# Kernel tuning notes

Hardware: AMD Instinct MI355X
Metric: run time of the kernel (lower is better)

The kernel has to match this reference:

```python
import jax, jax.numpy as jnp
import numpy as np

B, L, D, H, NL, EXP = 8, 1024, 512, 8, 6, 4
DH = D // H
DF = D * EXP
EPS = 1e-3  # keras LayerNormalization default epsilon
NEG = -1e9  # keras Softmax mask adder for float32


def _ln(x, g, b):
    m = jnp.mean(x, axis=-1, keepdims=True)
    v = jnp.mean(jnp.square(x - m), axis=-1, keepdims=True)
    return (x - m) * jax.lax.rsqrt(v + EPS) * g + b


def _pos_emb(L, D):
    pos = jnp.arange(L, dtype=jnp.float32)[:, None]          # [L,1]
    i = jnp.arange(D // 2, dtype=jnp.float32)[None, :]        # [1,D/2]
    inv = jnp.power(10000.0, -2.0 * i / D)
    # original concatenates sin block then cos block along feature axis
    return jnp.concatenate([jnp.sin(pos * inv), jnp.cos(pos * inv)], axis=-1)  # [L,D]


def setup_inputs() -> dict:
    key = jax.random.key(0)
    ks = jax.random.split(key, 16)
    glorot = lambda k, shape: jax.random.uniform(
        k, shape, jnp.float32, -1.0, 1.0) * jnp.sqrt(6.0 / (shape[-2] + shape[-1]))
    return {
        "x": jax.random.normal(ks[0], (B, L, D), jnp.float32),
        "lengths": jax.random.randint(ks[1], (B,), L // 2, L + 1).astype(jnp.int32),
        "Wq": glorot(ks[2], (NL, D, D)),
        "Wk": glorot(ks[3], (NL, D, D)),
        "Wv": glorot(ks[4], (NL, D, D)),
        "Wo": glorot(ks[5], (NL, D, D)),
        "ln1_g": jnp.ones((NL, D), jnp.float32),
        "ln1_b": jnp.zeros((NL, D), jnp.float32),
        "ln2_g": jnp.ones((NL, D), jnp.float32),
        "ln2_b": jnp.zeros((NL, D), jnp.float32),
        "w1": glorot(ks[6], (NL, D, DF)),
        "b1": jnp.zeros((NL, DF), jnp.float32),
        "w2": glorot(ks[7], (NL, DF, D)),
        "b2": jnp.zeros((NL, D), jnp.float32),
    }


def _forward(x, mask_bias, Wq, Wk, Wv, Wo, ln1_g, ln1_b, ln2_g, ln2_b, w1, b1, w2, b2):
    x = x + _pos_emb(L, D)[None, :, :]
    scale = 1.0 / jnp.sqrt(jnp.float32(DH))

    def layer(x, p):
        wq, wk, wv, wo, g1, be1, g2, be2, fw1, fb1, fw2, fb2 = p
        h = _ln(x, g1, be1)
        split = lambda t: t.reshape(B, L, H, DH).transpose(0, 2, 1, 3)  # [B,H,L,DH]
        q, k, v = split(h @ wq), split(h @ wk), split(h @ wv)
        scores = jnp.einsum("bhqd,bhkd->bhqk", q, k) * scale + mask_bias
        attn = jax.nn.softmax(scores, axis=-1)
        o = jnp.einsum("bhqk,bhkd->bhqd", attn, v)
        o = o.transpose(0, 2, 1, 3).reshape(B, L, D) @ wo
        x = x + o  # dropout is identity at inference
        h2 = _ln(x, g2, be2)
        ffn = jax.nn.relu(h2 @ fw1 + fb1) @ fw2 + fb2
        return x + ffn, None

    x, _ = jax.lax.scan(layer, x, (Wq, Wk, Wv, Wo, ln1_g, ln1_b, ln2_g, ln2_b, w1, b1, w2, b2))
    return x


def reference(x, lengths, Wq, Wk, Wv, Wo, ln1_g, ln1_b, ln2_g, ln2_b, w1, b1, w2, b2):
    mask = (jnp.arange(L)[None, :] < lengths[:, None]).astype(jnp.float32)  # [B,L]
    mask_bias = (1.0 - mask)[:, None, None, :] * NEG                        # [B,1,1,L]
    return _forward(x, mask_bias, Wq, Wk, Wv, Wo, ln1_g, ln1_b, ln2_g, ln2_b, w1, b1, w2, b2)
```

## Files before the change

### kernel.cpp

```cpp
#include <hip/hip_runtime.h>
#include <cstdint>
#include <cstddef>

#define Bz 8
#define Lz 1024
#define Dz 512
#define Hz 8
#define NLz 6
#define DFz 2048
#define Mz (Bz*Lz)

typedef short bf16x8 __attribute__((ext_vector_type(8)));
typedef float f32x4  __attribute__((ext_vector_type(4)));

__device__ __forceinline__ short f2bf(float f) {
    unsigned u = __builtin_bit_cast(unsigned, f);
    u = (u + 0x7fff + ((u >> 16) & 1)) >> 16;
    return (short)u;
}

__device__ __forceinline__ float exp2_fast(float x) {
#if __has_builtin(__builtin_amdgcn_exp2f)
    return __builtin_amdgcn_exp2f(x);
#else
    return exp2f(x);
#endif
}

#define GLD16(gp, lp) __builtin_amdgcn_global_load_lds( \
    (const __attribute__((address_space(1))) void*)(gp), \
    (__attribute__((address_space(3))) void*)(lp), 16, 0, 0)

__global__ __launch_bounds__(256) void posadd_kernel(const float* __restrict__ x,
                                                     float* __restrict__ y) {
    int idx = blockIdx.x * 256 + threadIdx.x;
    int d   = idx & (Dz - 1);
    int pos = (idx >> 9) & (Lz - 1);
    int i2  = (d < Dz/2) ? d : d - Dz/2;
    float inv = __expf(-0.03597789207f * (float)i2);
    float a = (float)pos * inv;
    float pe = (d < Dz/2) ? sinf(a) : cosf(a);
    y[idx] = x[idx] + pe;
}

__global__ __launch_bounds__(256) void ln_kernel(const float* __restrict__ x,
                                                 const float* __restrict__ g,
                                                 const float* __restrict__ b,
                                                 short* __restrict__ out) {
    int row = blockIdx.x;
    int t = threadIdx.x;
    const float* xr = x + (size_t)row * Dz;
    float v0 = xr[t], v1 = xr[t + 256];
    float s = v0 + v1;
    #pragma unroll
    for (int off = 32; off; off >>= 1) s += __shfl_xor(s, off, 64);
    __shared__ float red[4];
    int w = t >> 6, l = t & 63;
    if (l == 0) red[w] = s;
    __syncthreads();
    float m = (red[0] + red[1] + red[2] + red[3]) * (1.0f / Dz);
    float d0 = v0 - m, d1 = v1 - m;
    float s2 = d0 * d0 + d1 * d1;
    #pragma unroll
    for (int off = 32; off; off >>= 1) s2 += __shfl_xor(s2, off, 64);
    __syncthreads();
    if (l == 0) red[w] = s2;
    __syncthreads();
    float var = (red[0] + red[1] + red[2] + red[3]) * (1.0f / Dz);
    float rs = rsqrtf(var + 1e-3f);
    out[(size_t)row * Dz + t]       = f2bf(d0 * rs * g[t] + b[t]);
    out[(size_t)row * Dz + t + 256] = f2bf(d1 * rs * g[t + 256] + b[t + 256]);
}

__global__ __launch_bounds__(256) void transpose_bf16_kernel(const float* __restrict__ src,
                                                             short* __restrict__ dst,
                                                             int K, int N,
                                                             long srcLS, long dstLS, int rowOff) {
    __shared__ float tile[32][33];
    int tx = threadIdx.x & 31, ty = threadIdx.x >> 5;
    int bx = blockIdx.x, by = blockIdx.y, z = blockIdx.z;
    const float* s = src + (size_t)z * srcLS;
    short* d = dst + (size_t)z * dstLS;
    #pragma unroll
    for (int i = 0; i < 4; i++)
        tile[ty + i * 8][tx] = s[(size_t)(by * 32 + ty + i * 8) * N + bx * 32 + tx];
    __syncthreads();
    #pragma unroll
    for (int i = 0; i < 4; i++)
        d[(size_t)(rowOff + bx * 32 + ty + i * 8) * K + by * 32 + tx] = f2bf(tile[tx][ty + i * 8]);
}

__global__ __launch_bounds__(256) void vtrans_kernel(const short* __restrict__ qkv,
                                                     short* __restrict__ vbt) {
    int lt = blockIdx.x, bh = blockIdx.y;
    int b = bh >> 3, h = bh & 7;
    __shared__ short tile[64][72];
    int t = threadIdx.x;
    int l = t >> 2, c4 = t & 3;
    #pragma unroll
    for (int p = 0; p < 2; p++) {
        int dd = (c4 + p * 4) * 8;
        *(uint4*)&tile[l][dd] =
            *(const uint4*)(qkv + ((size_t)(b * Lz + lt * 64 + l)) * 1536 + 1024 + h * 64 + dd);
    }
    __syncthreads();
    int d = t >> 2;
    #pragma unroll
    for (int p = 0; p < 2; p++) {
        int lc = (c4 + p * 4) * 8;
        union { uint4 u; short s[8]; } o;
        #pragma unroll
        for (int j = 0; j < 8; j++) o.s[j] = tile[lc + j][d];
        *(uint4*)(vbt + ((size_t)(bh * 64 + d)) * Lz + lt * 64 + lc) = o.u;
    }
}

template<int MODE, int TN>
__global__ __launch_bounds__(256, (TN == 64) ? 4 : 2)
void gemm_bt(const short* __restrict__ A,
             const short* __restrict__ Bt,
             short* __restrict__ outb,
             float* __restrict__ outf,
             const float* __restrict__ bias,
             int M, int N, int K) {
    constexpr int NI = TN / 32;
    __shared__ __attribute__((aligned(16))) short As[128 * 32];
    __shared__ __attribute__((aligned(16))) short Bs[TN * 32];
    int t = threadIdx.x;
    int m0 = blockIdx.x * 128, n0 = blockIdx.y * TN;
    int w = t >> 6, l = t & 63;
    int wm = (w >> 1) * 64, wn = (w & 1) * (TN / 2);
    int lr = l & 15, lq = l >> 4;
    f32x4 acc[4][NI] = {};
    int ra0 = t >> 2, ca0 = (t & 3) * 8;
    int ra1 = (t + 256) >> 2;
    for (int kk = 0; kk < K; kk += 32) {
        GLD16(A + (size_t)(m0 + ra0) * K + kk + ca0, As + t * 8);
        GLD16(A + (size_t)(m0 + ra1) * K + kk + ca0, As + (t + 256) * 8);
        GLD16(Bt + (size_t)(n0 + ra0) * K + kk + ca0, Bs + t * 8);
        if constexpr (TN == 128)
            GLD16(Bt + (size_t)(n0 + ra1) * K + kk + ca0, Bs + (t + 256) * 8);
        __syncthreads();
        bf16x8 af[4], bfr[NI];
        #pragma unroll
        for (int i = 0; i < 4; i++)  af[i]  = *(const bf16x8*)(As + (wm + i * 16 + lr) * 32 + lq * 8);
        #pragma unroll
        for (int i = 0; i < NI; i++) bfr[i] = *(const bf16x8*)(Bs + (wn + i * 16 + lr) * 32 + lq * 8);
        #pragma unroll
        for (int mi = 0; mi < 4; mi++)
            #pragma unroll
            for (int ni = 0; ni < NI; ni++)
                acc[mi][ni] = __builtin_amdgcn_mfma_f32_16x16x32_bf16(af[mi], bfr[ni], acc[mi][ni], 0, 0, 0);
        __syncthreads();
    }
    #pragma unroll
    for (int mi = 0; mi < 4; mi++)
        #pragma unroll
        for (int ni = 0; ni < NI; ni++) {
            int col = n0 + wn + ni * 16 + lr;
            float bv = (MODE == 2 || MODE == 3) ? bias[col] : 0.0f;
            #pragma unroll
            for (int r = 0; r < 4; r++) {
                int row = m0 + wm + mi * 16 + lq * 4 + r;
                size_t idx = (size_t)row * N + col;
                float v = acc[mi][ni][r];
                if (MODE == 0)      outb[idx] = f2bf(v);
                else if (MODE == 1) outf[idx] += v;
                else if (MODE == 2) outb[idx] = f2bf(fmaxf(v + bv, 0.0f));
                else                outf[idx] += v + bv;
            }
        }
}

__device__ __forceinline__ void attn_frag(f32x4* sacc, const float* biask,
                                          float* mr, float* lsum, f32x4* oacc,
                                          short* Pw, const short* Vs,
                                          int lr, int lq, bf16x8 onesf) {
    const float SC2 = 0.18033688f;
    float p[8][4];
    #pragma unroll
    for (int r = 0; r < 4; r++) {
        float mx = -1e30f;
        #pragma unroll
        for (int kt = 0; kt < 8; kt++) {
            p[kt][r] = sacc[kt][r] * SC2 + biask[kt];
            mx = fmaxf(mx, p[kt][r]);
        }
        mx = fmaxf(mx, __shfl_xor(mx, 1, 64));
        mx = fmaxf(mx, __shfl_xor(mx, 2, 64));
        mx = fmaxf(mx, __shfl_xor(mx, 4, 64));
        mx = fmaxf(mx, __shfl_xor(mx, 8, 64));
        float mn = fmaxf(mr[r], mx);
        float alpha = exp2_fast(mr[r] - mn);
        mr[r] = mn;
        #pragma unroll
        for (int kt = 0; kt < 8; kt++)
            p[kt][r] = exp2_fast(p[kt][r] - mn);
        lsum[r] *= alpha;
        #pragma unroll
        for (int ni = 0; ni < 4; ni++) oacc[ni][r] *= alpha;
    }
    #pragma unroll
    for (int kt = 0; kt < 8; kt++)
        #pragma unroll
        for (int r = 0; r < 4; r++)
            Pw[(lq * 4 + r) * 136 + kt * 16 + lr] = f2bf(p[kt][r]);
    f32x4 sums = {};
    #pragma unroll
    for (int c = 0; c < 4; c++) {
        bf16x8 pf = *(const bf16x8*)(Pw + lr * 136 + c * 32 + lq * 8);
        sums = __builtin_amdgcn_mfma_f32_16x16x32_bf16(pf, onesf, sums, 0, 0, 0);
        #pragma unroll
        for (int ni = 0; ni < 4; ni++) {
            bf16x8 vf = *(const bf16x8*)(Vs + (ni * 16 + lr) * 136 + c * 32 + lq * 8);
            oacc[ni] = __builtin_amdgcn_mfma_f32_16x16x32_bf16(pf, vf, oacc[ni], 0, 0, 0);
        }
    }
    #pragma unroll
    for (int r = 0; r < 4; r++) lsum[r] += sums[r];
}

__global__ __launch_bounds__(256, 2) void attn_kernel(const short* __restrict__ qkv,
                                                      const short* __restrict__ vbt,
                                                      const int* __restrict__ lengths,
                                                      short* __restrict__ o) {
    __shared__ __attribute__((aligned(16))) short Ks[128 * 72];
    __shared__ __attribute__((aligned(16))) short Vs[64 * 136];
    __shared__ __attribute__((aligned(16))) short Ps[4][16 * 136];
    int qt = blockIdx.x;
    int bh = blockIdx.y;
    int b = bh >> 3, h = bh & 7;
    int len = lengths[b];
    int t = threadIdx.x, w = t >> 6, l = t & 63;
    int lr = l & 15, lq = l >> 4;

    const short* q0 = qkv + (size_t)(b * Lz + qt * 128 + w * 32 + lr) * 1536 + h * 64 + lq * 8;
    bf16x8 qf0a = *(const bf16x8*)(q0);
    bf16x8 qf0b = *(const bf16x8*)(q0 + 32);
    bf16x8 qf1a = *(const bf16x8*)(q0 + 16 * 1536);
    bf16x8 qf1b = *(const bf16x8*)(q0 + 16 * 1536 + 32);

    int kkey = t >> 3, kd8 = (t & 7) * 8;
    int vd = t >> 4, vk8 = (t & 15) * 8;
    const short* kbaseg = qkv + (size_t)(b * Lz) * 1536 + 512 + h * 64;
    const short* vbaseg = vbt + (size_t)(bh * 64) * Lz;

    float mr0[4] = {-1e30f, -1e30f, -1e30f, -1e30f}, ls0[4] = {0.f, 0.f, 0.f, 0.f};
    float mr1[4] = {-1e30f, -1e30f, -1e30f, -1e30f}, ls1[4] = {0.f, 0.f, 0.f, 0.f};
    f32x4 oacc0[4] = {}, oacc1[4] = {};
    bf16x8 onesf = {0x3F80, 0x3F80, 0x3F80, 0x3F80, 0x3F80, 0x3F80, 0x3F80, 0x3F80};

    uint4 kreg[4], vreg[4];
    #pragma unroll
    for (int i = 0; i < 4; i++)
        kreg[i] = *(const uint4*)(kbaseg + (size_t)(i * 32 + kkey) * 1536 + kd8);

    short* Pw = &Ps[w][0];
    int ntiles = (len + 127) >> 7;
    for (int tix = 0; tix < ntiles; tix++) {
        int k0 = tix << 7;
        __syncthreads();
        #pragma unroll
        for (int i = 0; i < 4; i++)
            *(uint4*)(Ks + (i * 32 + kkey) * 72 + kd8) = kreg[i];
        __syncthreads();
        #pragma unroll
        for (int i = 0; i < 4; i++)
            vreg[i] = *(const uint4*)(vbaseg + (size_t)(i * 16 + vd) * Lz + k0 + vk8);
        f32x4 sacc[8] = {};
        #pragma unroll
        for (int kt = 0; kt < 8; kt++) {
            bf16x8 kf0 = *(const bf16x8*)(Ks + (kt * 16 + lr) * 72 + lq * 8);
            bf16x8 kf1 = *(const bf16x8*)(Ks + (kt * 16 + lr) * 72 + 32 + lq * 8);
            sacc[kt] = __builtin_amdgcn_mfma_f32_16x16x32_bf16(qf0a, kf0, sacc[kt], 0, 0, 0);
            sacc[kt] = __builtin_amdgcn_mfma_f32_16x16x32_bf16(qf0b, kf1, sacc[kt], 0, 0, 0);
        }
        if (tix + 1 < ntiles) {
            #pragma unroll
            for (int i = 0; i < 4; i++)
                kreg[i] = *(const uint4*)(kbaseg + (size_t)(k0 + 128 + i * 32 + kkey) * 1536 + kd8);
        }
        #pragma unroll
        for (int i = 0; i < 4; i++)
            *(uint4*)(Vs + (i * 16 + vd) * 136 + vk8) = vreg[i];
        float biask[8];
        #pragma unroll
        for (int kt = 0; kt < 8; kt++)
            biask[kt] = ((k0 + kt * 16 + lr) < len) ? 0.0f : -1e30f;
        __syncthreads();
        attn_frag(sacc, biask, mr0, ls0, oacc0, Pw, Vs, lr, lq, onesf);
        #pragma unroll
        for (int kt = 0; kt < 8; kt++) {
            bf16x8 kf0 = *(const bf16x8*)(Ks + (kt * 16 + lr) * 72 + lq * 8);
            bf16x8 kf1 = *(const bf16x8*)(Ks + (kt * 16 + lr) * 72 + 32 + lq * 8);
            f32x4 s2 = {};
            s2 = __builtin_amdgcn_mfma_f32_16x16x32_bf16(qf1a, kf0, s2, 0, 0, 0);
            s2 = __builtin_amdgcn_mfma_f32_16x16x32_bf16(qf1b, kf1, s2, 0, 0, 0);
            sacc[kt] = s2;
        }
        attn_frag(sacc, biask, mr1, ls1, oacc1, Pw, Vs, lr, lq, onesf);
    }
    #pragma unroll
    for (int ni = 0; ni < 4; ni++)
        #pragma unroll
        for (int r = 0; r < 4; r++) {
            int q = qt * 128 + w * 32 + lq * 4 + r;
            size_t base = (size_t)(b * Lz + q) * Dz + h * 64 + ni * 16 + lr;
            o[base]             = f2bf(oacc0[ni][r] / ls0[r]);
            o[base + 16 * Dz]   = f2bf(oacc1[ni][r] / ls1[r]);
        }
}

extern "C" void kernel_launch(void* const* d_in, const int* in_sizes, int n_in,
                              void* d_out, int out_size, void* d_ws, size_t ws_size,
                              hipStream_t stream) {
    const float* x_in    = (const float*)d_in[0];
    const int*   lengths = (const int*)d_in[1];
    const float* Wq   = (const float*)d_in[2];
    const float* Wk   = (const float*)d_in[3];
    const float* Wv   = (const float*)d_in[4];
    const float* Wo   = (const float*)d_in[5];
    const float* ln1g = (const float*)d_in[6];
    const float* ln1b = (const float*)d_in[7];
    const float* ln2g = (const float*)d_in[8];
    const float* ln2b = (const float*)d_in[9];
    const float* w1   = (const float*)d_in[10];
    const float* b1   = (const float*)d_in[11];
    const float* w2   = (const float*)d_in[12];
    const float* b2   = (const float*)d_in[13];

    size_t off = 0;
    auto alloc = [&](size_t bytes) {
        void* p = (char*)d_ws + off;
        off += (bytes + 255) & ~(size_t)255;
        return p;
    };
    float* x_work = (float*)alloc((size_t)Mz * Dz * 4);
    short* hbuf   = (short*)alloc((size_t)Mz * Dz * 2);
    short* qkvb   = (short*)alloc((size_t)Mz * 1536 * 2);
    short* f1b    = (short*)alloc((size_t)Mz * DFz * 2);
    short* vbt    = (short*)alloc((size_t)Bz * Hz * 64 * Lz * 2);
    short* wqkvT  = (short*)alloc((size_t)NLz * 1536 * Dz * 2);
    short* woT    = (short*)alloc((size_t)NLz * Dz * Dz * 2);
    short* w1T    = (short*)alloc((size_t)NLz * DFz * Dz * 2);
    short* w2T    = (short*)alloc((size_t)NLz * Dz * DFz * 2);

    dim3 tb(256);
    transpose_bf16_kernel<<<dim3(16, 16, NLz), tb, 0, stream>>>(Wq, wqkvT, Dz, Dz, (long)Dz*Dz, (long)1536*Dz, 0);
    transpose_bf16_kernel<<<dim3(16, 16, NLz), tb, 0, stream>>>(Wk, wqkvT, Dz, Dz, (long)Dz*Dz, (long)1536*Dz, 512);
    transpose_bf16_kernel<<<dim3(16, 16, NLz), tb, 0, stream>>>(Wv, wqkvT, Dz, Dz, (long)Dz*Dz, (long)1536*Dz, 1024);
    transpose_bf16_kernel<<<dim3(16, 16, NLz), tb, 0, stream>>>(Wo, woT, Dz, Dz, (long)Dz*Dz, (long)Dz*Dz, 0);
    transpose_bf16_kernel<<<dim3(64, 16, NLz), tb, 0, stream>>>(w1, w1T, Dz, DFz, (long)Dz*DFz, (long)DFz*Dz, 0);
    transpose_bf16_kernel<<<dim3(16, 64, NLz), tb, 0, stream>>>(w2, w2T, DFz, Dz, (long)DFz*Dz, (long)Dz*DFz, 0);

    posadd_kernel<<<dim3(Mz * Dz / 256), tb, 0, stream>>>(x_in, x_work);

    for (int lyr = 0; lyr < NLz; lyr++) {
        const short* wqkvL = wqkvT + (size_t)lyr * 1536 * Dz;
        const short* woL   = woT   + (size_t)lyr * Dz * Dz;
        const short* w1L   = w1T   + (size_t)lyr * DFz * Dz;
        const short* w2L   = w2T   + (size_t)lyr * Dz * DFz;

        ln_kernel<<<dim3(Mz), tb, 0, stream>>>(x_work, ln1g + lyr * Dz, ln1b + lyr * Dz, hbuf);
        gemm_bt<0,128><<<dim3(Mz/128, 1536/128), tb, 0, stream>>>(hbuf, wqkvL, qkvb, nullptr, nullptr, Mz, 1536, Dz);
        vtrans_kernel<<<dim3(Lz/64, Bz*Hz), tb, 0, stream>>>(qkvb, vbt);
        attn_kernel<<<dim3(Lz/128, Bz*Hz), tb, 0, stream>>>(qkvb, vbt, lengths, hbuf);
        gemm_bt<1,64><<<dim3(Mz/128, Dz/64), tb, 0, stream>>>(hbuf, woL, nullptr, x_work, nullptr, Mz, Dz, Dz);
        ln_kernel<<<dim3(Mz), tb, 0, stream>>>(x_work, ln2g + lyr * Dz, ln2b + lyr * Dz, hbuf);
        gemm_bt<2,128><<<dim3(Mz/128, DFz/128), tb, 0, stream>>>(hbuf, w1L, f1b, nullptr, b1 + lyr * DFz, Mz, DFz, Dz);
        gemm_bt<3,64><<<dim3(Mz/128, Dz/64), tb, 0, stream>>>(f1b, w2L, nullptr, x_work, b2 + lyr * Dz, Mz, Dz, DFz);
    }

    hipMemcpyAsync(d_out, x_work, (size_t)Mz * Dz * 4, hipMemcpyDeviceToDevice, stream);
}
```

Measured before the change: 1.202 ms.

## Split-K output GEMMs with atomics and shrink attention query tiles for occupancy

The Wo and FFN-down GEMMs gain a split-K template parameter set to 2. Each K half accumulates into the fp32 residual with atomicAdd, and only the first split adds the bias. The attention kernel now handles 64 queries per block instead of 128, uses a flattened 1D grid with qt-major ordering, and raises the occupancy bound to 4. It also aliases the P scratch buffer onto the K tile and prefetches V into registers alongside K. The aim is more blocks and better overlap of loads with compute on the narrow-N GEMMs and in attention, paid for with atomic traffic, nondeterministic float summation order, and K/V tiles reloaded by twice as many blocks.

```diff
diff --git a/kernel.cpp b/kernel.cpp
--- a/kernel.cpp
+++ b/kernel.cpp
@@ -115,7 +115,7 @@
     }
 }
 
-template<int MODE, int TN>
+template<int MODE, int TN, int SPLIT>
 __global__ __launch_bounds__(256, (TN == 64) ? 4 : 2)
 void gemm_bt(const short* __restrict__ A,
              const short* __restrict__ Bt,
@@ -128,13 +128,15 @@
     __shared__ __attribute__((aligned(16))) short Bs[TN * 32];
     int t = threadIdx.x;
     int m0 = blockIdx.x * 128, n0 = blockIdx.y * TN;
+    int z = (SPLIT > 1) ? blockIdx.z : 0;
+    int kBeg = z * (K / SPLIT), kEnd = kBeg + K / SPLIT;
     int w = t >> 6, l = t & 63;
     int wm = (w >> 1) * 64, wn = (w & 1) * (TN / 2);
     int lr = l & 15, lq = l >> 4;
     f32x4 acc[4][NI] = {};
     int ra0 = t >> 2, ca0 = (t & 3) * 8;
     int ra1 = (t + 256) >> 2;
-    for (int kk = 0; kk < K; kk += 32) {
+    for (int kk = kBeg; kk < kEnd; kk += 32) {
         GLD16(A + (size_t)(m0 + ra0) * K + kk + ca0, As + t * 8);
         GLD16(A + (size_t)(m0 + ra1) * K + kk + ca0, As + (t + 256) * 8);
         GLD16(Bt + (size_t)(n0 + ra0) * K + kk + ca0, Bs + t * 8);
@@ -165,9 +167,15 @@
                 size_t idx = (size_t)row * N + col;
                 float v = acc[mi][ni][r];
                 if (MODE == 0)      outb[idx] = f2bf(v);
-                else if (MODE == 1) outf[idx] += v;
-                else if (MODE == 2) outb[idx] = f2bf(fmaxf(v + bv, 0.0f));
-                else                outf[idx] += v + bv;
+                else if (MODE == 1) {
+                    if (SPLIT > 1) atomicAdd(outf + idx, v);
+                    else           outf[idx] += v;
+                } else if (MODE == 2) outb[idx] = f2bf(fmaxf(v + bv, 0.0f));
+                else {
+                    float vb = v + ((z == 0) ? bv : 0.0f);
+                    if (SPLIT > 1) atomicAdd(outf + idx, vb);
+                    else           outf[idx] += vb;
+                }
             }
         }
 }
@@ -220,94 +228,80 @@
     for (int r = 0; r < 4; r++) lsum[r] += sums[r];
 }
 
-__global__ __launch_bounds__(256, 2) void attn_kernel(const short* __restrict__ qkv,
+__global__ __launch_bounds__(256, 4) void attn_kernel(const short* __restrict__ qkv,
                                                       const short* __restrict__ vbt,
                                                       const int* __restrict__ lengths,
                                                       short* __restrict__ o) {
     __shared__ __attribute__((aligned(16))) short Ks[128 * 72];
     __shared__ __attribute__((aligned(16))) short Vs[64 * 136];
-    __shared__ __attribute__((aligned(16))) short Ps[4][16 * 136];
-    int qt = blockIdx.x;
-    int bh = blockIdx.y;
+    int id = blockIdx.x;
+    int qt = id >> 6;
+    int bh = id & 63;
     int b = bh >> 3, h = bh & 7;
     int len = lengths[b];
     int t = threadIdx.x, w = t >> 6, l = t & 63;
     int lr = l & 15, lq = l >> 4;
 
-    const short* q0 = qkv + (size_t)(b * Lz + qt * 128 + w * 32 + lr) * 1536 + h * 64 + lq * 8;
-    bf16x8 qf0a = *(const bf16x8*)(q0);
-    bf16x8 qf0b = *(const bf16x8*)(q0 + 32);
-    bf16x8 qf1a = *(const bf16x8*)(q0 + 16 * 1536);
-    bf16x8 qf1b = *(const bf16x8*)(q0 + 16 * 1536 + 32);
+    const short* q0 = qkv + (size_t)(b * Lz + qt * 64 + w * 16 + lr) * 1536 + h * 64 + lq * 8;
+    bf16x8 qf0 = *(const bf16x8*)(q0);
+    bf16x8 qf1 = *(const bf16x8*)(q0 + 32);
 
     int kkey = t >> 3, kd8 = (t & 7) * 8;
     int vd = t >> 4, vk8 = (t & 15) * 8;
     const short* kbaseg = qkv + (size_t)(b * Lz) * 1536 + 512 + h * 64;
     const short* vbaseg = vbt + (size_t)(bh * 64) * Lz;
 
-    float mr0[4] = {-1e30f, -1e30f, -1e30f, -1e30f}, ls0[4] = {0.f, 0.f, 0.f, 0.f};
-    float mr1[4] = {-1e30f, -1e30f, -1e30f, -1e30f}, ls1[4] = {0.f, 0.f, 0.f, 0.f};
-    f32x4 oacc0[4] = {}, oacc1[4] = {};
+    float mr[4] = {-1e30f, -1e30f, -1e30f, -1e30f}, ls[4] = {0.f, 0.f, 0.f, 0.f};
+    f32x4 oacc[4] = {};
     bf16x8 onesf = {0x3F80, 0x3F80, 0x3F80, 0x3F80, 0x3F80, 0x3F80, 0x3F80, 0x3F80};
 
     uint4 kreg[4], vreg[4];
     #pragma unroll
-    for (int i = 0; i < 4; i++)
+    for (int i = 0; i < 4; i++) {
         kreg[i] = *(const uint4*)(kbaseg + (size_t)(i * 32 + kkey) * 1536 + kd8);
-
-    short* Pw = &Ps[w][0];
+        vreg[i] = *(const uint4*)(vbaseg + (size_t)(i * 16 + vd) * Lz + vk8);
+    }
+
+    short* Pw = Ks + w * 2304;
     int ntiles = (len + 127) >> 7;
     for (int tix = 0; tix < ntiles; tix++) {
         int k0 = tix << 7;
         __syncthreads();
         #pragma unroll
-        for (int i = 0; i < 4; i++)
+        for (int i = 0; i < 4; i++) {
             *(uint4*)(Ks + (i * 32 + kkey) * 72 + kd8) = kreg[i];
-        __syncthreads();
-        #pragma unroll
-        for (int i = 0; i < 4; i++)
-            vreg[i] = *(const uint4*)(vbaseg + (size_t)(i * 16 + vd) * Lz + k0 + vk8);
+            *(uint4*)(Vs + (i * 16 + vd) * 136 + vk8) = vreg[i];
+        }
+        __syncthreads();
         f32x4 sacc[8] = {};
         #pragma unroll
         for (int kt = 0; kt < 8; kt++) {
             bf16x8 kf0 = *(const bf16x8*)(Ks + (kt * 16 + lr) * 72 + lq * 8);
             bf16x8 kf1 = *(const bf16x8*)(Ks + (kt * 16 + lr) * 72 + 32 + lq * 8);
-            sacc[kt] = __builtin_amdgcn_mfma_f32_16x16x32_bf16(qf0a, kf0, sacc[kt], 0, 0, 0);
-            sacc[kt] = __builtin_amdgcn_mfma_f32_16x16x32_bf16(qf0b, kf1, sacc[kt], 0, 0, 0);
+            sacc[kt] = __builtin_amdgcn_mfma_f32_16x16x32_bf16(qf0, kf0, sacc[kt], 0, 0, 0);
+            sacc[kt] = __builtin_amdgcn_mfma_f32_16x16x32_bf16(qf1, kf1, sacc[kt], 0, 0, 0);
         }
         if (tix + 1 < ntiles) {
+            int kn = k0 + 128;
             #pragma unroll
-            for (int i = 0; i < 4; i++)
-                kreg[i] = *(const uint4*)(kbaseg + (size_t)(k0 + 128 + i * 32 + kkey) * 1536 + kd8);
-        }
-        #pragma unroll
-        for (int i = 0; i < 4; i++)
-            *(uint4*)(Vs + (i * 16 + vd) * 136 + vk8) = vreg[i];
+            for (int i = 0; i < 4; i++) {
+                kreg[i] = *(const uint4*)(kbaseg + (size_t)(kn + i * 32 + kkey) * 1536 + kd8);
+                vreg[i] = *(const uint4*)(vbaseg + (size_t)(i * 16 + vd) * Lz + kn + vk8);
+            }
+        }
         float biask[8];
         #pragma unroll
         for (int kt = 0; kt < 8; kt++)
             biask[kt] = ((k0 + kt * 16 + lr) < len) ? 0.0f : -1e30f;
         __syncthreads();
-        attn_frag(sacc, biask, mr0, ls0, oacc0, Pw, Vs, lr, lq, onesf);
-        #pragma unroll
-        for (int kt = 0; kt < 8; kt++) {
-            bf16x8 kf0 = *(const bf16x8*)(Ks + (kt * 16 + lr) * 72 + lq * 8);
-            bf16x8 kf1 = *(const bf16x8*)(Ks + (kt * 16 + lr) * 72 + 32 + lq * 8);
-            f32x4 s2 = {};
-            s2 = __builtin_amdgcn_mfma_f32_16x16x32_bf16(qf1a, kf0, s2, 0, 0, 0);
-            s2 = __builtin_amdgcn_mfma_f32_16x16x32_bf16(qf1b, kf1, s2, 0, 0, 0);
-            sacc[kt] = s2;
-        }
-        attn_frag(sacc, biask, mr1, ls1, oacc1, Pw, Vs, lr, lq, onesf);
+        attn_frag(sacc, biask, mr, ls, oacc, Pw, Vs, lr, lq, onesf);
     }
     #pragma unroll
     for (int ni = 0; ni < 4; ni++)
         #pragma unroll
         for (int r = 0; r < 4; r++) {
-            int q = qt * 128 + w * 32 + lq * 4 + r;
-            size_t base = (size_t)(b * Lz + q) * Dz + h * 64 + ni * 16 + lr;
-            o[base]             = f2bf(oacc0[ni][r] / ls0[r]);
-            o[base + 16 * Dz]   = f2bf(oacc1[ni][r] / ls1[r]);
+            int q = qt * 64 + w * 16 + lq * 4 + r;
+            o[(size_t)(b * Lz + q) * Dz + h * 64 + ni * 16 + lr] = f2bf(oacc[ni][r] / ls[r]);
         }
 }
 
@@ -362,13 +356,13 @@
         const short* w2L   = w2T   + (size_t)lyr * Dz * DFz;
 
         ln_kernel<<<dim3(Mz), tb, 0, stream>>>(x_work, ln1g + lyr * Dz, ln1b + lyr * Dz, hbuf);
-        gemm_bt<0,128><<<dim3(Mz/128, 1536/128), tb, 0, stream>>>(hbuf, wqkvL, qkvb, nullptr, nullptr, Mz, 1536, Dz);
+        gemm_bt<0,128,1><<<dim3(Mz/128, 1536/128), tb, 0, stream>>>(hbuf, wqkvL, qkvb, nullptr, nullptr, Mz, 1536, Dz);
         vtrans_kernel<<<dim3(Lz/64, Bz*Hz), tb, 0, stream>>>(qkvb, vbt);
-        attn_kernel<<<dim3(Lz/128, Bz*Hz), tb, 0, stream>>>(qkvb, vbt, lengths, hbuf);
-        gemm_bt<1,64><<<dim3(Mz/128, Dz/64), tb, 0, stream>>>(hbuf, woL, nullptr, x_work, nullptr, Mz, Dz, Dz);
+        attn_kernel<<<dim3((Lz/64) * Bz * Hz), tb, 0, stream>>>(qkvb, vbt, lengths, hbuf);
+        gemm_bt<1,64,2><<<dim3(Mz/128, Dz/64, 2), tb, 0, stream>>>(hbuf, woL, nullptr, x_work, nullptr, Mz, Dz, Dz);
         ln_kernel<<<dim3(Mz), tb, 0, stream>>>(x_work, ln2g + lyr * Dz, ln2b + lyr * Dz, hbuf);
-        gemm_bt<2,128><<<dim3(Mz/128, DFz/128), tb, 0, stream>>>(hbuf, w1L, f1b, nullptr, b1 + lyr * DFz, Mz, DFz, Dz);
-        gemm_bt<3,64><<<dim3(Mz/128, Dz/64), tb, 0, stream>>>(f1b, w2L, nullptr, x_work, b2 + lyr * Dz, Mz, Dz, DFz);
+        gemm_bt<2,128,1><<<dim3(Mz/128, DFz/128), tb, 0, stream>>>(hbuf, w1L, f1b, nullptr, b1 + lyr * DFz, Mz, DFz, Dz);
+        gemm_bt<3,64,2><<<dim3(Mz/128, Dz/64, 2), tb, 0, stream>>>(f1b, w2L, nullptr, x_work, b2 + lyr * Dz, Mz, Dz, DFz);
     }
 
     hipMemcpyAsync(d_out, x_work, (size_t)Mz * Dz * 4, hipMemcpyDeviceToDevice, stream);
```

Result: slower. 1.506 ms (+25.3%).
